# Kernel optimization log

Measured on AMD Instinct MI355X. Metric: run time of the kernel, lower is better.

The kernel has to match this reference:

```python
import jax, jax.numpy as jnp
import numpy as np

B, S, D = 8, 2048, 768
H1 = 512
EMBED_DIM = 768  # scale = sqrt(embed_dim)


def setup_inputs() -> dict:
    key = jax.random.key(0)
    ks = jax.random.split(key, 5)
    q = jax.random.normal(ks[0], (B, S, D), dtype=jnp.float32)
    k = jax.random.normal(ks[1], (B, S, D), dtype=jnp.float32)
    v = jax.random.normal(ks[2], (B, S, D), dtype=jnp.float32)
    W1 = jax.random.normal(ks[3], (D, H1), dtype=jnp.float32) * (1.0 / np.sqrt(D))
    b1 = jnp.zeros((H1,), dtype=jnp.float32)
    W2 = jax.random.normal(ks[4], (H1, 1), dtype=jnp.float32) * (1.0 / np.sqrt(H1))
    b2 = jnp.zeros((1,), dtype=jnp.float32)
    return {"q": q, "k": k, "v": v, "W1": W1, "b1": b1, "W2": W2, "b2": b2}


def reference(q, k, v, W1, b1, W2, b2):
    # MLP gate on v: fc2(tanh(fc1(v))) -> [B, S, 1] -> squeeze -> [B, S]
    g = jnp.tanh(v @ W1 + b1) @ W2 + b2          # [B, S, 1]
    g = g[..., 0][:, None, :]                    # unsqueeze(-2): [B, 1, S]

    # scores scaled by sqrt(seq_len) (q.shape[1]), as in the original
    scores = jnp.einsum("bqd,bkd->bqk", q, k) / jnp.sqrt(
        jnp.asarray(q.shape[1], dtype=q.dtype))  # [B, S, S]

    # first softmax over dim=1 (column-wise over query axis)
    s = jax.nn.softmax(scores, axis=1)           # [B, S, S]

    # blend with column-mean, scale by sqrt(embed_dim)
    s_mean = jnp.mean(s, axis=1, keepdims=True)  # [B, 1, S]
    scale = jnp.sqrt(jnp.asarray(EMBED_DIM, dtype=q.dtype))
    attn_scores = (s * (1.0 - g) + s_mean * g) / scale

    # second softmax over last dim; dropout p=0 is identity
    attn_weights = jax.nn.softmax(attn_scores, axis=-1)

    attn_output = jnp.einsum("bqk,bkd->bqd", attn_weights, v) + q
    return attn_output, attn_weights
```

## Files before the change

kernel.cpp:

```cpp
#include <hip/hip_runtime.h>

#define BATCH 8
#define SEQ   2048
#define DIM   768
#define HID   512

typedef __attribute__((ext_vector_type(8))) short  short8;
typedef __attribute__((ext_vector_type(4))) float  f32x4;

__device__ __forceinline__ unsigned short f2bf(float f) {
  union { float f; unsigned u; } x; x.f = f;
  return (unsigned short)((x.u + 0x7FFFu + ((x.u >> 16) & 1u)) >> 16);
}
__device__ __forceinline__ float bf2f(unsigned short u) {
  union { unsigned u; float f; } x; x.u = ((unsigned)u) << 16;
  return x.f;
}
__device__ __forceinline__ void gll16(const void* g, void* l) {
  __builtin_amdgcn_global_load_lds(
      (const __attribute__((address_space(1))) void*)g,
      (__attribute__((address_space(3))) void*)l, 16, 0, 0);
}
__device__ __forceinline__ int swz2(int o) { return o ^ (((o >> 8) & 7) << 4); }
__device__ __forceinline__ int swz3(int o) { return o ^ (((o >> 7) & 7) << 4); }

template<int VAR>
__global__ __launch_bounds__(256)
void gemm_db(const unsigned short* __restrict__ Ab, const unsigned short* __restrict__ Bb,
             const float* __restrict__ bias, const float* __restrict__ W2,
             float* __restrict__ pg, const float* __restrict__ qres,
             float* __restrict__ Cf)
{
  constexpr int K      = (VAR == 2) ? SEQ : DIM;
  constexpr int NT     = K / 32;
  constexpr int APITCH = (VAR == 0) ? 4096 : (VAR == 1 ? DIM : SEQ);
  constexpr int BPITCH = (VAR == 0) ? DIM  : (VAR == 1 ? 4096 : SEQ);
  constexpr int GX     = (VAR == 0) ? 4 : (VAR == 1 ? 16 : 6);
  constexpr int GY     = (VAR == 0) ? 128 : 16;
  constexpr int NWG    = GX * GY * ((VAR == 0) ? 1 : 8);

  __shared__ __align__(16) unsigned short AsL[2 * 128 * 32];
  __shared__ __align__(16) unsigned short BsL[2 * 128 * 32];
  __shared__ float gred[(VAR == 0) ? 128 : 1][2];

  int wg = blockIdx.x;
  wg = (wg & 7) * (NWG >> 3) + (wg >> 3);
  const int bx = wg % GX;
  const int by = (wg / GX) % GY;
  const int z  = wg / (GX * GY);

  const int tid  = threadIdx.x;
  const int brow = by * 128;
  const int bcol = bx * 128;
  const int lane = tid & 63;
  const int wid  = tid >> 6;
  const int wr   = (wid >> 1) * 64;
  const int wc   = (wid & 1) * 64;
  const int lhi  = lane >> 4;
  const int llo  = lane & 15;

  const unsigned short* Asrc = Ab;
  const unsigned short* Bsrc = Bb;
  if constexpr (VAR == 1) { Asrc += (size_t)z * SEQ * DIM; Bsrc += (size_t)z * SEQ * 4096; }
  if constexpr (VAR == 2) { Asrc += (size_t)z * SEQ * SEQ; Bsrc += (size_t)z * DIM * SEQ; }
  Asrc += (size_t)brow * APITCH;
  Bsrc += (size_t)bcol * BPITCH;

  f32x4 acc[4][4];
  #pragma unroll
  for (int m = 0; m < 4; ++m)
    #pragma unroll
    for (int n = 0; n < 4; ++n)
      acc[m][n] = (f32x4)(0.0f);

  auto stage = [&](int buf, int k0) {
    #pragma unroll
    for (int i = 0; i < 2; ++i) {
      int ob = wid * 2048 + i * 1024;
      int o  = ob + lane * 16;
      int a  = swz2(o);
      gll16((const char*)Asrc + (size_t)(a >> 6) * (APITCH * 2) + (size_t)k0 * 2 + (a & 63),
            (char*)AsL + buf * 8192 + ob);
    }
    #pragma unroll
    for (int i = 0; i < 2; ++i) {
      int ob = wid * 2048 + i * 1024;
      int o  = ob + lane * 16;
      int a  = swz2(o);
      gll16((const char*)Bsrc + (size_t)(a >> 6) * (BPITCH * 2) + (size_t)k0 * 2 + (a & 63),
            (char*)BsL + buf * 8192 + ob);
    }
  };

  stage(0, 0);
  for (int t = 0; t < NT; ++t) {
    if (t + 1 < NT) {
      stage((t + 1) & 1, (t + 1) * 32);
      asm volatile("s_waitcnt vmcnt(4)" ::: "memory");
    } else {
      asm volatile("s_waitcnt vmcnt(0)" ::: "memory");
    }
    __builtin_amdgcn_s_barrier();
    __builtin_amdgcn_sched_barrier(0);

    const int bb = (t & 1) * 8192;
    short8 af[4], bfr[4];
    #pragma unroll
    for (int m = 0; m < 4; ++m) {
      int a = (wr + m * 16 + llo) * 64 + lhi * 16;
      af[m] = *(const short8*)((const char*)AsL + bb + swz2(a));
    }
    #pragma unroll
    for (int n = 0; n < 4; ++n) {
      int a = (wc + n * 16 + llo) * 64 + lhi * 16;
      bfr[n] = *(const short8*)((const char*)BsL + bb + swz2(a));
    }
    #pragma unroll
    for (int m = 0; m < 4; ++m)
      #pragma unroll
      for (int n = 0; n < 4; ++n)
        acc[m][n] = __builtin_amdgcn_mfma_f32_16x16x32_bf16(af[m], bfr[n], acc[m][n], 0, 0, 0);

    __builtin_amdgcn_sched_barrier(0);
    __builtin_amdgcn_s_barrier();
    __builtin_amdgcn_sched_barrier(0);
  }

  if constexpr (VAR == 0) {
    #pragma unroll
    for (int m = 0; m < 4; ++m) {
      #pragma unroll
      for (int r = 0; r < 4; ++r) {
        int lrow = wr + m * 16 + lhi * 4 + r;
        float part = 0.f;
        #pragma unroll
        for (int n = 0; n < 4; ++n) {
          int colg = bcol + wc + n * 16 + llo;
          float t = tanhf(acc[m][n][r] + bias[colg]);
          part += t * W2[colg];
        }
        part += __shfl_xor(part, 1);
        part += __shfl_xor(part, 2);
        part += __shfl_xor(part, 4);
        part += __shfl_xor(part, 8);
        if (llo == 0) gred[lrow][wid & 1] = part;
      }
    }
    __syncthreads();
    if (tid < 128)
      pg[(size_t)bx * 16384 + brow + tid] = gred[tid][0] + gred[tid][1];
  }
  if constexpr (VAR == 1) {
    const float rs = 0.02209708691207961f;
    unsigned short* C16 = reinterpret_cast<unsigned short*>(Cf);
    #pragma unroll
    for (int m = 0; m < 4; ++m)
      #pragma unroll
      for (int r = 0; r < 4; ++r) {
        size_t R = (size_t)z * SEQ + (brow + wr + m * 16 + lhi * 4 + r);
        #pragma unroll
        for (int n = 0; n < 4; ++n) {
          int colg = bcol + wc + n * 16 + llo;
          C16[R * 4096 + colg] = f2bf(acc[m][n][r] * rs);
        }
      }
  }
  if constexpr (VAR == 2) {
    float* C = Cf + (size_t)z * SEQ * DIM;
    const float* Q = qres + (size_t)z * SEQ * DIM;
    #pragma unroll
    for (int m = 0; m < 4; ++m)
      #pragma unroll
      for (int r = 0; r < 4; ++r) {
        int rowg = brow + wr + m * 16 + lhi * 4 + r;
        #pragma unroll
        for (int n = 0; n < 4; ++n) {
          int colg = bcol + wc + n * 16 + llo;
          C[(size_t)rowg * DIM + colg] = acc[m][n][r] + Q[(size_t)rowg * DIM + colg];
        }
      }
  }
}

__global__ __launch_bounds__(256)
void gemm_slow(const float* __restrict__ Wf, const float* __restrict__ Vf,
               const float* __restrict__ qres, float* __restrict__ Cf)
{
  __shared__ __align__(16) unsigned short AsL[128 * 64];
  __shared__ __align__(16) unsigned short BsL[128 * 32];

  const int tid  = threadIdx.x;
  const int z    = blockIdx.z;
  const int brow = blockIdx.y * 128;
  const int bcol = blockIdx.x * 128;
  const int lane = tid & 63;
  const int wid  = tid >> 6;
  const int wr   = (wid >> 1) * 64;
  const int wc   = (wid & 1) * 64;
  const int lhi  = lane >> 4;
  const int llo  = lane & 15;

  const float* AsrcF = Wf + (size_t)z * SEQ * SEQ + (size_t)brow * SEQ;
  const float* BsrcF = Vf + (size_t)z * SEQ * DIM;

  f32x4 acc[4][4];
  #pragma unroll
  for (int m = 0; m < 4; ++m)
    #pragma unroll
    for (int n = 0; n < 4; ++n)
      acc[m][n] = (f32x4)(0.0f);

  for (int k0 = 0; k0 < SEQ; k0 += 32) {
    #pragma unroll
    for (int i = 0; i < 4; ++i) {
      int ob = wid * 4096 + i * 1024;
      int o  = ob + lane * 16;
      int a  = swz3(o);
      gll16((const char*)AsrcF + (size_t)(a >> 7) * (SEQ * 4) + (size_t)k0 * 4 + (a & 127),
            (char*)AsL + ob);
    }
    {
      int n4 = (tid & 31) << 2;
      int kb = (tid >> 5) << 2;
      float4 r0 = *(const float4*)(BsrcF + (size_t)(k0 + kb + 0) * DIM + bcol + n4);
      float4 r1 = *(const float4*)(BsrcF + (size_t)(k0 + kb + 1) * DIM + bcol + n4);
      float4 r2 = *(const float4*)(BsrcF + (size_t)(k0 + kb + 2) * DIM + bcol + n4);
      float4 r3 = *(const float4*)(BsrcF + (size_t)(k0 + kb + 3) * DIM + bcol + n4);
      float a0[4] = {r0.x, r0.y, r0.z, r0.w};
      float a1[4] = {r1.x, r1.y, r1.z, r1.w};
      float a2[4] = {r2.x, r2.y, r2.z, r2.w};
      float a3[4] = {r3.x, r3.y, r3.z, r3.w};
      #pragma unroll
      for (int jj = 0; jj < 4; ++jj) {
        unsigned lo = (__float_as_uint(a0[jj]) >> 16) | (__float_as_uint(a1[jj]) & 0xFFFF0000u);
        unsigned hi = (__float_as_uint(a2[jj]) >> 16) | (__float_as_uint(a3[jj]) & 0xFFFF0000u);
        int ol = (n4 + jj) * 64 + kb * 2;
        *(uint2*)((char*)BsL + swz2(ol)) = make_uint2(lo, hi);
      }
    }
    __syncthreads();

    short8 af[4], bfr[4];
    #pragma unroll
    for (int m = 0; m < 4; ++m) {
      int row = wr + m * 16 + llo;
      int a0i = row * 128 + lhi * 32;
      f32x4 x = *(const f32x4*)((const char*)AsL + swz3(a0i));
      f32x4 y = *(const f32x4*)((const char*)AsL + swz3(a0i + 16));
      union { unsigned u[4]; short8 s; } r;
      r.u[0] = (__float_as_uint(x[0]) >> 16) | (__float_as_uint(x[1]) & 0xFFFF0000u);
      r.u[1] = (__float_as_uint(x[2]) >> 16) | (__float_as_uint(x[3]) & 0xFFFF0000u);
      r.u[2] = (__float_as_uint(y[0]) >> 16) | (__float_as_uint(y[1]) & 0xFFFF0000u);
      r.u[3] = (__float_as_uint(y[2]) >> 16) | (__float_as_uint(y[3]) & 0xFFFF0000u);
      af[m] = r.s;
    }
    #pragma unroll
    for (int n = 0; n < 4; ++n) {
      int a = (wc + n * 16 + llo) * 64 + lhi * 16;
      bfr[n] = *(const short8*)((const char*)BsL + swz2(a));
    }
    #pragma unroll
    for (int m = 0; m < 4; ++m)
      #pragma unroll
      for (int n = 0; n < 4; ++n)
        acc[m][n] = __builtin_amdgcn_mfma_f32_16x16x32_bf16(af[m], bfr[n], acc[m][n], 0, 0, 0);
    __syncthreads();
  }

  float* C = Cf + (size_t)z * SEQ * DIM;
  const float* Q = qres + (size_t)z * SEQ * DIM;
  #pragma unroll
  for (int m = 0; m < 4; ++m)
    #pragma unroll
    for (int r = 0; r < 4; ++r) {
      int rowg = brow + wr + m * 16 + lhi * 4 + r;
      #pragma unroll
      for (int n = 0; n < 4; ++n) {
        int colg = bcol + wc + n * 16 + llo;
        C[(size_t)rowg * DIM + colg] = acc[m][n][r] + Q[(size_t)rowg * DIM + colg];
      }
    }
}

__global__ __launch_bounds__(256)
void prepack(const float* __restrict__ q, const float* __restrict__ k,
             const float* __restrict__ v, unsigned short* __restrict__ qb,
             unsigned short* __restrict__ wsl)
{
  const int NT = (BATCH * SEQ * DIM) / 4;
  for (int i = blockIdx.x * 256 + threadIdx.x; i < NT; i += 2048 * 256) {
    int e = i * 4;
    float4 qv = *(const float4*)(q + e);
    float4 kv = *(const float4*)(k + e);
    float4 vv = *(const float4*)(v + e);
    ushort4 qo; qo.x = f2bf(qv.x); qo.y = f2bf(qv.y); qo.z = f2bf(qv.z); qo.w = f2bf(qv.w);
    ushort4 ko; ko.x = f2bf(kv.x); ko.y = f2bf(kv.y); ko.z = f2bf(kv.z); ko.w = f2bf(kv.w);
    ushort4 vo; vo.x = f2bf(vv.x); vo.y = f2bf(vv.y); vo.z = f2bf(vv.z); vo.w = f2bf(vv.w);
    *(ushort4*)(qb + e) = qo;
    int r = e / DIM, c = e % DIM;
    size_t off = (size_t)r * 4096 + 2048 + c;
    *(ushort4*)(wsl + off) = ko;
    *(ushort4*)(wsl + off + DIM) = vo;
  }
}

__global__ __launch_bounds__(256)
void transpose_f32_bf16(const float* __restrict__ src, unsigned short* __restrict__ dst,
                        int R, int C)
{
  __shared__ unsigned short T[64][65];
  const float* s = src + (size_t)blockIdx.z * R * C;
  unsigned short* d = dst + (size_t)blockIdx.z * R * C;
  int r0 = blockIdx.y * 64, c0 = blockIdx.x * 64;
  int tr = threadIdx.x >> 6, tc = threadIdx.x & 63;
  #pragma unroll
  for (int j = 0; j < 16; ++j) {
    int row = j * 4 + tr;
    T[row][tc] = f2bf(s[(size_t)(r0 + row) * C + c0 + tc]);
  }
  __syncthreads();
  #pragma unroll
  for (int j = 0; j < 16; ++j) {
    int row = j * 4 + tr;
    d[(size_t)(c0 + row) * R + r0 + tc] = T[tc][row];
  }
}

__global__ void g_combine(const float* __restrict__ pg, const float* __restrict__ b2,
                          float* __restrict__ g)
{
  int i = blockIdx.x * 256 + threadIdx.x;
  g[i] = b2[0] + pg[i] + pg[16384 + i] + pg[2 * 16384 + i] + pg[3 * 16384 + i];
}

__global__ __launch_bounds__(256)
void colstat_part(const unsigned short* __restrict__ sc, float* __restrict__ pl)
{
  const int gc = blockIdx.x * 256 + threadIdx.x;
  const int b = gc >> 11, c = gc & 2047;
  const unsigned short* p = sc + (size_t)b * SEQ * 4096 + c;
  const int q0 = blockIdx.y * 128;
  float l = 0.f;
  #pragma unroll 4
  for (int qq = q0; qq < q0 + 128; ++qq) l += __expf(bf2f(p[(size_t)qq * 4096]));
  pl[blockIdx.y * 16384 + gc] = l;
}

__global__ void colstat_comb(const float* __restrict__ pl, float* __restrict__ lcol)
{
  int gc = blockIdx.x * 256 + threadIdx.x;
  float l = 0.f;
  #pragma unroll
  for (int ch = 0; ch < 16; ++ch) l += pl[ch * 16384 + gc];
  lcol[gc] = l;
}

template<bool FAST>
__global__ __launch_bounds__(256)
void rowpass(float* __restrict__ w, const float* __restrict__ lcol,
             const float* __restrict__ gg, unsigned short* __restrict__ wb)
{
  const size_t row = blockIdx.x;
  const int b = (int)(row >> 11);
  const unsigned short* p = (const unsigned short*)w + row * 4096;
  float* wrow = w + row * 2048;
  const int c0 = threadIdx.x * 8;
  const float* lc = lcol + (b << 11);
  const float* gb = gg + (b << 11);

  unsigned short xs[8];
  *(ushort4*)&xs[0] = *(const ushort4*)(p + c0);
  *(ushort4*)&xs[4] = *(const ushort4*)(p + c0 + 4);
  float ls[8], gs[8];
  *(float4*)&ls[0] = *(const float4*)(lc + c0);
  *(float4*)&ls[4] = *(const float4*)(lc + c0 + 4);
  *(float4*)&gs[0] = *(const float4*)(gb + c0);
  *(float4*)&gs[4] = *(const float4*)(gb + c0 + 4);

  float e[8];
  float psum = 0.f;
  #pragma unroll
  for (int j = 0; j < 8; ++j) {
    float s = __expf(bf2f(xs[j])) / ls[j];
    float t = (s * (1.f - gs[j]) + gs[j] * (1.f / 2048.f)) * 0.03608439182435161f;
    float ev = __expf(t);
    e[j] = ev;
    psum += ev;
  }
  #pragma unroll
  for (int off = 1; off < 64; off <<= 1) psum += __shfl_xor(psum, off);
  __shared__ float red[4];
  if ((threadIdx.x & 63) == 0) red[threadIdx.x >> 6] = psum;
  __syncthreads();
  float inv = 1.f / (red[0] + red[1] + red[2] + red[3]);
  float4 o0, o1;
  o0.x = e[0] * inv; o0.y = e[1] * inv; o0.z = e[2] * inv; o0.w = e[3] * inv;
  o1.x = e[4] * inv; o1.y = e[5] * inv; o1.z = e[6] * inv; o1.w = e[7] * inv;
  *(float4*)(wrow + c0) = o0;
  *(float4*)(wrow + c0 + 4) = o1;
  if constexpr (FAST) {
    ushort4 b0, b1v;
    b0.x = f2bf(o0.x); b0.y = f2bf(o0.y); b0.z = f2bf(o0.z); b0.w = f2bf(o0.w);
    b1v.x = f2bf(o1.x); b1v.y = f2bf(o1.y); b1v.z = f2bf(o1.z); b1v.w = f2bf(o1.w);
    *(ushort4*)(wb + row * 2048 + c0) = b0;
    *(ushort4*)(wb + row * 2048 + c0 + 4) = b1v;
  }
}

extern "C" void kernel_launch(void* const* d_in, const int* in_sizes, int n_in,
                              void* d_out, int out_size, void* d_ws, size_t ws_size,
                              hipStream_t stream)
{
  (void)in_sizes; (void)n_in; (void)out_size;
  const float* q  = (const float*)d_in[0];
  const float* k  = (const float*)d_in[1];
  const float* v  = (const float*)d_in[2];
  const float* W1 = (const float*)d_in[3];
  const float* b1 = (const float*)d_in[4];
  const float* W2 = (const float*)d_in[5];
  const float* b2 = (const float*)d_in[6];

  float* out0 = (float*)d_out;
  float* wbuf = out0 + (size_t)BATCH * SEQ * DIM;
  unsigned short* wsl = (unsigned short*)wbuf;
  unsigned short* qb  = (unsigned short*)out0;

  float* g    = (float*)d_ws;
  float* lcol = g + 16384;
  float* pg   = lcol + 16384;
  float* pl   = pg + 65536;
  unsigned short* W1T = (unsigned short*)(pl + 262144);
  unsigned short* vT  = (unsigned short*)((char*)d_ws + 2228224);
  unsigned short* wb  = vT + (size_t)12582912;
  const bool fast = ws_size >= 94502912ull;

  prepack<<<2048, 256, 0, stream>>>(q, k, v, qb, wsl);
  transpose_f32_bf16<<<dim3(8, 12, 1), 256, 0, stream>>>(W1, W1T, 768, 512);
  if (fast)
    transpose_f32_bf16<<<dim3(12, 32, 8), 256, 0, stream>>>(v, vT, 2048, 768);

  gemm_db<0><<<512, 256, 0, stream>>>(wsl + 2816, W1T, b1, W2, pg, nullptr, nullptr);
  g_combine<<<64, 256, 0, stream>>>(pg, b2, g);

  gemm_db<1><<<2048, 256, 0, stream>>>(qb, wsl + 2048, nullptr, nullptr, nullptr, nullptr, wbuf);

  colstat_part<<<dim3(64, 16), 256, 0, stream>>>(wsl, pl);
  colstat_comb<<<64, 256, 0, stream>>>(pl, lcol);

  if (fast) {
    rowpass<true><<<16384, 256, 0, stream>>>(wbuf, lcol, g, wb);
    gemm_db<2><<<768, 256, 0, stream>>>(wb, vT, nullptr, nullptr, nullptr, q, out0);
  } else {
    rowpass<false><<<16384, 256, 0, stream>>>(wbuf, lcol, g, nullptr);
    gemm_slow<<<dim3(6, 16, 8), 256, 0, stream>>>(wbuf, v, q, out0);
  }
}
```

Baseline: 311.2 us.

## Replace QK^T and PV GEMMs with 256x256-tile 8-wave pipelined kernel

Result: faster. 274.9 us (-11.7%).

```diff
diff --git a/kernel.cpp b/kernel.cpp
--- a/kernel.cpp
+++ b/kernel.cpp
@@ -8,6 +8,10 @@
 typedef __attribute__((ext_vector_type(8))) short  short8;
 typedef __attribute__((ext_vector_type(4))) float  f32x4;
 
+#define BAR()   asm volatile("s_barrier" ::: "memory")
+#define WAITL0() asm volatile("s_waitcnt lgkmcnt(0)" ::: "memory")
+#define VMC(n)  asm volatile("s_waitcnt vmcnt(" #n ")" ::: "memory")
+
 __device__ __forceinline__ unsigned short f2bf(float f) {
   union { float f; unsigned u; } x; x.f = f;
   return (unsigned short)((x.u + 0x7FFFu + ((x.u >> 16) & 1u)) >> 16);
@@ -25,29 +29,192 @@
 __device__ __forceinline__ int swz3(int o) { return o ^ (((o >> 7) & 7) << 4); }
 
 template<int VAR>
+__global__ __launch_bounds__(512, 2)
+void gemm8(const unsigned short* __restrict__ Ap, const unsigned short* __restrict__ Bp,
+           const float* __restrict__ qres, float* __restrict__ Cf)
+{
+  constexpr int K     = (VAR == 1) ? DIM : SEQ;
+  constexpr int NT    = K / 64;
+  constexpr int NITER = NT / 2;
+  constexpr int APB   = (VAR == 1) ? DIM * 2 : SEQ * 2;
+  constexpr int BPB   = (VAR == 1) ? 8192    : SEQ * 2;
+  constexpr int GX    = (VAR == 1) ? 8 : 3;
+  constexpr int GY    = 8;
+  constexpr int NWG   = GX * GY * BATCH;
+
+  __shared__ __align__(16) unsigned char LDS[131072];
+
+  int wg = ((blockIdx.x & 7) * (NWG >> 3)) + ((int)blockIdx.x >> 3);
+  const int z  = wg / (GX * GY);
+  const int r2 = wg % (GX * GY);
+  const int by = r2 / GX;
+  const int bx = r2 % GX;
+  const int brow = by * 256, bcol = bx * 256;
+
+  const int tid  = threadIdx.x;
+  const int lane = tid & 63, wid = tid >> 6;
+  const int wm   = wid >> 2, wn = wid & 3;
+  const int lhi  = lane >> 4, llo = lane & 15;
+
+  const char* Abase;
+  const char* Bbase;
+  if constexpr (VAR == 1) {
+    Abase = (const char*)(Ap + (size_t)z * SEQ * DIM) + (size_t)brow * APB;
+    Bbase = (const char*)(Bp + (size_t)z * SEQ * 4096 + 2048) + (size_t)bcol * BPB;
+  } else {
+    Abase = (const char*)(Ap + (size_t)z * SEQ * SEQ) + (size_t)brow * APB;
+    Bbase = (const char*)(Bp + (size_t)z * (size_t)DIM * SEQ) + (size_t)bcol * BPB;
+  }
+
+  int sr[2], sk[2];
+  #pragma unroll
+  for (int c = 0; c < 2; ++c) {
+    int o = wid * 2048 + c * 1024 + lane * 16;
+    int a = swz3(o);
+    sr[c] = a >> 7; sk[c] = a & 127;
+  }
+  auto stA = [&](int buf, int hh, int t) {
+    #pragma unroll
+    for (int c = 0; c < 2; ++c)
+      gll16(Abase + (size_t)(hh * 128 + sr[c]) * APB + t * 128 + sk[c],
+            LDS + buf * 32768 + hh * 16384 + wid * 2048 + c * 1024);
+  };
+  auto stB = [&](int buf, int hh, int t) {
+    #pragma unroll
+    for (int c = 0; c < 2; ++c)
+      gll16(Bbase + (size_t)(hh * 128 + sr[c]) * BPB + t * 128 + sk[c],
+            LDS + 65536 + buf * 32768 + hh * 16384 + wid * 2048 + c * 1024);
+  };
+
+  f32x4 acc[8][4];
+  #pragma unroll
+  for (int m = 0; m < 8; ++m)
+    #pragma unroll
+    for (int n = 0; n < 4; ++n)
+      acc[m][n] = (f32x4)(0.0f);
+
+  stA(0, 0, 0); stA(0, 1, 0); stB(0, 0, 0); stB(0, 1, 0);
+  stB(1, 0, 1); stB(1, 1, 1);
+  VMC(4);
+  BAR();
+
+  auto ITER = [&](int i, bool last) {
+    #pragma unroll
+    for (int kk = 0; kk < 2; ++kk) {
+      const int buf = kk;
+      short8 aR[4][2], b0R[2][2], b1R[2][2];
+      #pragma unroll
+      for (int ph = 0; ph < 4; ++ph) {
+        const int h  = ph >> 1;
+        const int nh = (ph == 1 || ph == 2) ? 1 : 0;
+        if (ph == 0 || ph == 2) {
+          #pragma unroll
+          for (int fm = 0; fm < 4; ++fm)
+            #pragma unroll
+            for (int kh = 0; kh < 2; ++kh) {
+              int o = (wm * 128 + h * 64 + fm * 16 + llo) * 128 + kh * 64 + lhi * 16;
+              aR[fm][kh] = *(const short8*)(LDS + buf * 32768 + swz3(o));
+            }
+        }
+        if (ph == 0) {
+          #pragma unroll
+          for (int fn = 0; fn < 2; ++fn)
+            #pragma unroll
+            for (int kh = 0; kh < 2; ++kh) {
+              int o = (wn * 64 + fn * 16 + llo) * 128 + kh * 64 + lhi * 16;
+              b0R[fn][kh] = *(const short8*)(LDS + 65536 + buf * 32768 + swz3(o));
+            }
+        }
+        if (ph == 1) {
+          #pragma unroll
+          for (int fn = 0; fn < 2; ++fn)
+            #pragma unroll
+            for (int kh = 0; kh < 2; ++kh) {
+              int o = (wn * 64 + 32 + fn * 16 + llo) * 128 + kh * 64 + lhi * 16;
+              b1R[fn][kh] = *(const short8*)(LDS + 65536 + buf * 32768 + swz3(o));
+            }
+        }
+        const int P = kk * 4 + ph;
+        if      (P == 0) stA(1, 0, 2 * i + 1);
+        else if (P == 1) stA(1, 1, 2 * i + 1);
+        else if (P == 2) { if (!last) stB(0, 0, 2 * i + 2); }
+        else if (P == 3) { if (!last) stB(0, 1, 2 * i + 2); }
+        else if (P == 4) { if (!last) stA(0, 0, 2 * i + 2); }
+        else if (P == 5) { if (!last) stA(0, 1, 2 * i + 2); }
+        else if (P == 6) { if (!last) stB(1, 0, 2 * i + 3); }
+        else if (P == 7) { if (!last) stB(1, 1, 2 * i + 3); }
+        if (P == 3) { if (last) { VMC(0); } else { VMC(4); } }
+        if (P == 7) { if (!last) { VMC(4); } }
+        BAR();
+        WAITL0();
+        __builtin_amdgcn_sched_barrier(0);
+        __builtin_amdgcn_s_setprio(1);
+        #pragma unroll
+        for (int kh = 0; kh < 2; ++kh)
+          #pragma unroll
+          for (int fm = 0; fm < 4; ++fm)
+            #pragma unroll
+            for (int fn = 0; fn < 2; ++fn)
+              acc[h * 4 + fm][nh * 2 + fn] = __builtin_amdgcn_mfma_f32_16x16x32_bf16(
+                  aR[fm][kh], nh ? b1R[fn][kh] : b0R[fn][kh],
+                  acc[h * 4 + fm][nh * 2 + fn], 0, 0, 0);
+        __builtin_amdgcn_s_setprio(0);
+        BAR();
+      }
+    }
+  };
+
+  for (int i = 0; i < NITER - 1; ++i) ITER(i, false);
+  ITER(NITER - 1, true);
+
+  if constexpr (VAR == 1) {
+    const float rs = 0.02209708691207961f;
+    unsigned short* C16 = reinterpret_cast<unsigned short*>(Cf);
+    #pragma unroll
+    for (int FM = 0; FM < 8; ++FM)
+      #pragma unroll
+      for (int r = 0; r < 4; ++r) {
+        size_t R = (size_t)z * SEQ + (brow + wm * 128 + FM * 16 + lhi * 4 + r);
+        #pragma unroll
+        for (int FN = 0; FN < 4; ++FN) {
+          int col = bcol + wn * 64 + FN * 16 + llo;
+          C16[R * 4096 + col] = f2bf(acc[FM][FN][r] * rs);
+        }
+      }
+  }
+  if constexpr (VAR == 2) {
+    float* C = Cf + (size_t)z * SEQ * DIM;
+    const float* Q = qres + (size_t)z * SEQ * DIM;
+    #pragma unroll
+    for (int FM = 0; FM < 8; ++FM)
+      #pragma unroll
+      for (int r = 0; r < 4; ++r) {
+        int rowg = brow + wm * 128 + FM * 16 + lhi * 4 + r;
+        #pragma unroll
+        for (int FN = 0; FN < 4; ++FN) {
+          int colg = bcol + wn * 64 + FN * 16 + llo;
+          C[(size_t)rowg * DIM + colg] = acc[FM][FN][r] + Q[(size_t)rowg * DIM + colg];
+        }
+      }
+  }
+}
+
 __global__ __launch_bounds__(256)
-void gemm_db(const unsigned short* __restrict__ Ab, const unsigned short* __restrict__ Bb,
-             const float* __restrict__ bias, const float* __restrict__ W2,
-             float* __restrict__ pg, const float* __restrict__ qres,
-             float* __restrict__ Cf)
-{
-  constexpr int K      = (VAR == 2) ? SEQ : DIM;
-  constexpr int NT     = K / 32;
-  constexpr int APITCH = (VAR == 0) ? 4096 : (VAR == 1 ? DIM : SEQ);
-  constexpr int BPITCH = (VAR == 0) ? DIM  : (VAR == 1 ? 4096 : SEQ);
-  constexpr int GX     = (VAR == 0) ? 4 : (VAR == 1 ? 16 : 6);
-  constexpr int GY     = (VAR == 0) ? 128 : 16;
-  constexpr int NWG    = GX * GY * ((VAR == 0) ? 1 : 8);
+void gemm_gate(const unsigned short* __restrict__ Ab, const unsigned short* __restrict__ Bb,
+               const float* __restrict__ bias, const float* __restrict__ W2,
+               float* __restrict__ pg)
+{
+  constexpr int K = DIM, NT = K / 32, APITCH = 4096, BPITCH = DIM;
+  constexpr int GX = 4, NWG = 512;
 
   __shared__ __align__(16) unsigned short AsL[2 * 128 * 32];
   __shared__ __align__(16) unsigned short BsL[2 * 128 * 32];
-  __shared__ float gred[(VAR == 0) ? 128 : 1][2];
+  __shared__ float gred[128][2];
 
   int wg = blockIdx.x;
   wg = (wg & 7) * (NWG >> 3) + (wg >> 3);
   const int bx = wg % GX;
-  const int by = (wg / GX) % GY;
-  const int z  = wg / (GX * GY);
+  const int by = wg / GX;
 
   const int tid  = threadIdx.x;
   const int brow = by * 128;
@@ -59,12 +226,8 @@
   const int lhi  = lane >> 4;
   const int llo  = lane & 15;
 
-  const unsigned short* Asrc = Ab;
-  const unsigned short* Bsrc = Bb;
-  if constexpr (VAR == 1) { Asrc += (size_t)z * SEQ * DIM; Bsrc += (size_t)z * SEQ * 4096; }
-  if constexpr (VAR == 2) { Asrc += (size_t)z * SEQ * SEQ; Bsrc += (size_t)z * DIM * SEQ; }
-  Asrc += (size_t)brow * APITCH;
-  Bsrc += (size_t)bcol * BPITCH;
+  const unsigned short* Asrc = Ab + (size_t)brow * APITCH;
+  const unsigned short* Bsrc = Bb + (size_t)bcol * BPITCH;
 
   f32x4 acc[4][4];
   #pragma unroll
@@ -77,16 +240,14 @@
     #pragma unroll
     for (int i = 0; i < 2; ++i) {
       int ob = wid * 2048 + i * 1024;
-      int o  = ob + lane * 16;
-      int a  = swz2(o);
+      int a  = swz2(ob + lane * 16);
       gll16((const char*)Asrc + (size_t)(a >> 6) * (APITCH * 2) + (size_t)k0 * 2 + (a & 63),
             (char*)AsL + buf * 8192 + ob);
     }
     #pragma unroll
     for (int i = 0; i < 2; ++i) {
       int ob = wid * 2048 + i * 1024;
-      int o  = ob + lane * 16;
-      int a  = swz2(o);
+      int a  = swz2(ob + lane * 16);
       gll16((const char*)Bsrc + (size_t)(a >> 6) * (BPITCH * 2) + (size_t)k0 * 2 + (a & 63),
             (char*)BsL + buf * 8192 + ob);
     }
@@ -96,11 +257,11 @@
   for (int t = 0; t < NT; ++t) {
     if (t + 1 < NT) {
       stage((t + 1) & 1, (t + 1) * 32);
-      asm volatile("s_waitcnt vmcnt(4)" ::: "memory");
+      VMC(4);
     } else {
-      asm volatile("s_waitcnt vmcnt(0)" ::: "memory");
-    }
-    __builtin_amdgcn_s_barrier();
+      VMC(0);
+    }
+    BAR();
     __builtin_amdgcn_sched_barrier(0);
 
     const int bb = (t & 1) * 8192;
@@ -122,64 +283,32 @@
         acc[m][n] = __builtin_amdgcn_mfma_f32_16x16x32_bf16(af[m], bfr[n], acc[m][n], 0, 0, 0);
 
     __builtin_amdgcn_sched_barrier(0);
-    __builtin_amdgcn_s_barrier();
+    BAR();
     __builtin_amdgcn_sched_barrier(0);
   }
 
-  if constexpr (VAR == 0) {
-    #pragma unroll
-    for (int m = 0; m < 4; ++m) {
-      #pragma unroll
-      for (int r = 0; r < 4; ++r) {
-        int lrow = wr + m * 16 + lhi * 4 + r;
-        float part = 0.f;
-        #pragma unroll
-        for (int n = 0; n < 4; ++n) {
-          int colg = bcol + wc + n * 16 + llo;
-          float t = tanhf(acc[m][n][r] + bias[colg]);
-          part += t * W2[colg];
-        }
-        part += __shfl_xor(part, 1);
-        part += __shfl_xor(part, 2);
-        part += __shfl_xor(part, 4);
-        part += __shfl_xor(part, 8);
-        if (llo == 0) gred[lrow][wid & 1] = part;
+  #pragma unroll
+  for (int m = 0; m < 4; ++m) {
+    #pragma unroll
+    for (int r = 0; r < 4; ++r) {
+      int lrow = wr + m * 16 + lhi * 4 + r;
+      float part = 0.f;
+      #pragma unroll
+      for (int n = 0; n < 4; ++n) {
+        int colg = bcol + wc + n * 16 + llo;
+        float t = tanhf(acc[m][n][r] + bias[colg]);
+        part += t * W2[colg];
       }
-    }
-    __syncthreads();
-    if (tid < 128)
-      pg[(size_t)bx * 16384 + brow + tid] = gred[tid][0] + gred[tid][1];
-  }
-  if constexpr (VAR == 1) {
-    const float rs = 0.02209708691207961f;
-    unsigned short* C16 = reinterpret_cast<unsigned short*>(Cf);
-    #pragma unroll
-    for (int m = 0; m < 4; ++m)
-      #pragma unroll
-      for (int r = 0; r < 4; ++r) {
-        size_t R = (size_t)z * SEQ + (brow + wr + m * 16 + lhi * 4 + r);
-        #pragma unroll
-        for (int n = 0; n < 4; ++n) {
-          int colg = bcol + wc + n * 16 + llo;
-          C16[R * 4096 + colg] = f2bf(acc[m][n][r] * rs);
-        }
-      }
-  }
-  if constexpr (VAR == 2) {
-    float* C = Cf + (size_t)z * SEQ * DIM;
-    const float* Q = qres + (size_t)z * SEQ * DIM;
-    #pragma unroll
-    for (int m = 0; m < 4; ++m)
-      #pragma unroll
-      for (int r = 0; r < 4; ++r) {
-        int rowg = brow + wr + m * 16 + lhi * 4 + r;
-        #pragma unroll
-        for (int n = 0; n < 4; ++n) {
-          int colg = bcol + wc + n * 16 + llo;
-          C[(size_t)rowg * DIM + colg] = acc[m][n][r] + Q[(size_t)rowg * DIM + colg];
-        }
-      }
-  }
+      part += __shfl_xor(part, 1);
+      part += __shfl_xor(part, 2);
+      part += __shfl_xor(part, 4);
+      part += __shfl_xor(part, 8);
+      if (llo == 0) gred[lrow][wid & 1] = part;
+    }
+  }
+  __syncthreads();
+  if (tid < 128)
+    pg[(size_t)bx * 16384 + brow + tid] = gred[tid][0] + gred[tid][1];
 }
 
 __global__ __launch_bounds__(256)
@@ -214,8 +343,7 @@
     #pragma unroll
     for (int i = 0; i < 4; ++i) {
       int ob = wid * 4096 + i * 1024;
-      int o  = ob + lane * 16;
-      int a  = swz3(o);
+      int a  = swz3(ob + lane * 16);
       gll16((const char*)AsrcF + (size_t)(a >> 7) * (SEQ * 4) + (size_t)k0 * 4 + (a & 127),
             (char*)AsL + ob);
     }
@@ -439,17 +567,17 @@
   if (fast)
     transpose_f32_bf16<<<dim3(12, 32, 8), 256, 0, stream>>>(v, vT, 2048, 768);
 
-  gemm_db<0><<<512, 256, 0, stream>>>(wsl + 2816, W1T, b1, W2, pg, nullptr, nullptr);
+  gemm_gate<<<512, 256, 0, stream>>>(wsl + 2816, W1T, b1, W2, pg);
   g_combine<<<64, 256, 0, stream>>>(pg, b2, g);
 
-  gemm_db<1><<<2048, 256, 0, stream>>>(qb, wsl + 2048, nullptr, nullptr, nullptr, nullptr, wbuf);
+  gemm8<1><<<512, 512, 0, stream>>>(qb, wsl, nullptr, wbuf);
 
   colstat_part<<<dim3(64, 16), 256, 0, stream>>>(wsl, pl);
   colstat_comb<<<64, 256, 0, stream>>>(pl, lcol);
 
   if (fast) {
     rowpass<true><<<16384, 256, 0, stream>>>(wbuf, lcol, g, wb);
-    gemm_db<2><<<768, 256, 0, stream>>>(wb, vT, nullptr, nullptr, nullptr, q, out0);
+    gemm8<2><<<192, 512, 0, stream>>>(wb, vT, q, out0);
   } else {
     rowpass<false><<<16384, 256, 0, stream>>>(wbuf, lcol, g, nullptr);
     gemm_slow<<<dim3(6, 16, 8), 256, 0, stream>>>(wbuf, v, q, out0);
```
